# Performance work log

Hardware: AMD Instinct MI355X
Metric: run time of the kernel (lower is better)

The kernel has to match this reference:

```python
import jax, jax.numpy as jnp
import numpy as np

H = 1024      # hidden_size
V = 32000     # output_size (vocab)
BOS = 1


def setup_inputs() -> dict:
    key = jax.random.key(0)
    ks = jax.random.split(key, 12)
    B, S, T = 16, 128, 128
    s = 1.0 / np.sqrt(H)
    return {
        "encoder_outputs": jax.random.normal(ks[0], (B, S, H), jnp.float32),
        "encoder_hidden": jax.random.normal(ks[1], (1, B, H), jnp.float32),
        "tgt_tensor": jax.random.randint(ks[2], (B, T), 0, V),
        # embedding table
        "emb": jax.random.normal(ks[3], (V, H), jnp.float32) * 0.02,
        # additive attention (d2l style: Linear(..., bias=False))
        "Wq": jax.random.uniform(ks[4], (H, H), jnp.float32, -s, s),
        "Wk": jax.random.uniform(ks[5], (H, H), jnp.float32, -s, s),
        "v_att": jax.random.uniform(ks[6], (H,), jnp.float32, -s, s),
        # GRU (input size 2H): PyTorch layout W_ih [3H, 2H] (r,z,n), W_hh [3H, H]
        "W_ih": jax.random.uniform(ks[7], (3 * H, 2 * H), jnp.float32, -s, s),
        "W_hh": jax.random.uniform(ks[8], (3 * H, H), jnp.float32, -s, s),
        "b_ih": jax.random.uniform(ks[9], (3 * H,), jnp.float32, -s, s),
        "b_hh": jax.random.uniform(ks[10], (3 * H,), jnp.float32, -s, s),
        # output linear
        "W_out": jax.random.uniform(ks[11], (V, H), jnp.float32, -s, s),
        "b_out": jnp.zeros((V,), jnp.float32),
    }


def _decode(encoder_outputs, encoder_hidden, tgt_tensor,
            emb, Wq, Wk, v_att, W_ih, W_hh, b_ih, b_hh, W_out, b_out):
    B, S, _ = encoder_outputs.shape
    # decoder inputs under teacher forcing: [BOS, tgt[:, :-1]]  -> [B, T]
    dec_in = jnp.concatenate(
        [jnp.full((B, 1), BOS, dtype=tgt_tensor.dtype), tgt_tensor[:, :-1]], axis=1)
    # precompute key projection once: [B, S, H]
    kproj = jnp.einsum('bsh,gh->bsg', encoder_outputs, Wk)

    def step(h, x_t):  # h: [B,H], x_t: [B]
        e = emb[x_t]                                   # [B, H]
        q = h @ Wq.T                                   # [B, H]
        feat = jnp.tanh(q[:, None, :] + kproj)         # [B, S, H]
        scores = jnp.einsum('bsh,h->bs', feat, v_att)  # [B, S]
        w = jax.nn.softmax(scores, axis=-1)            # [B, S]
        ctx = jnp.einsum('bs,bsh->bh', w, encoder_outputs)  # [B, H]
        x = jnp.concatenate([e, ctx], axis=-1)         # [B, 2H]
        gx = x @ W_ih.T + b_ih                         # [B, 3H]
        gh = h @ W_hh.T + b_hh                         # [B, 3H]
        gx_r, gx_z, gx_n = jnp.split(gx, 3, axis=-1)
        gh_r, gh_z, gh_n = jnp.split(gh, 3, axis=-1)
        r = jax.nn.sigmoid(gx_r + gh_r)
        z = jax.nn.sigmoid(gx_z + gh_z)
        n = jnp.tanh(gx_n + r * gh_n)
        h_new = (1.0 - z) * n + z * h                  # [B, H]
        logits = h_new @ W_out.T + b_out               # [B, V]
        return h_new, (logits, w)

    h0 = encoder_hidden[0]                             # [B, H]
    hT, (logits, attw) = jax.lax.scan(step, h0, dec_in.T)  # time-major scan
    logits = jnp.transpose(logits, (1, 0, 2))          # [B, T, V]
    attw = jnp.transpose(attw, (1, 0, 2))              # [B, T, S]
    log_probs = jax.nn.log_softmax(logits, axis=-1)
    return log_probs, hT[None], attw


def reference(encoder_outputs, encoder_hidden, tgt_tensor,
              emb, Wq, Wk, v_att, W_ih, W_hh, b_ih, b_hh, W_out, b_out):
    return _decode(encoder_outputs, encoder_hidden, tgt_tensor,
                   emb, Wq, Wk, v_att, W_ih, W_hh, b_ih, b_hh, W_out, b_out)
```

## Files before the change

### kernel.cpp

```cpp
#include <hip/hip_runtime.h>

typedef unsigned short u16;
using f32x4  = __attribute__((ext_vector_type(4))) float;
using bf16x8 = __attribute__((ext_vector_type(8))) __bf16;

__device__ __forceinline__ float bf2f(u16 s){ return __builtin_bit_cast(float, (unsigned)s << 16); }
__device__ __forceinline__ float bflo(unsigned u){ return __builtin_bit_cast(float, u << 16); }
__device__ __forceinline__ float bfhi(unsigned u){ return __builtin_bit_cast(float, u & 0xffff0000u); }
__device__ __forceinline__ u16 f2bf(float f){
  unsigned u = __builtin_bit_cast(unsigned, f);
  unsigned r = u + 0x7fffu + ((u >> 16) & 1u);
  return (u16)(r >> 16);
}
__device__ __forceinline__ unsigned pk2(float x, float y){
  unsigned ux = __builtin_bit_cast(unsigned, x) + 0x8000u;
  unsigned uy = __builtin_bit_cast(unsigned, y) + 0x8000u;
  return (ux >> 16) | (uy & 0xffff0000u);
}
__device__ __forceinline__ float tanh_f(float x){ float e = __expf(2.f*x); return 1.f - 2.f/(e + 1.f); }
__device__ __forceinline__ float sigm(float x){ return 1.f/(1.f + __expf(-x)); }
__device__ __forceinline__ f32x4 mfma16(bf16x8 a, bf16x8 b, f32x4 c){
  return __builtin_amdgcn_mfma_f32_16x16x32_bf16(a, b, c, 0, 0, 0);
}
__device__ __forceinline__ bf16x8 ldg8(const u16* p){
  return __builtin_bit_cast(bf16x8, *(const uint4*)p);
}
__device__ __forceinline__ bf16x8 cvt8(const float* p){
  float4 a = *(const float4*)p, b = *(const float4*)(p + 4);
  uint4 r; r.x = pk2(a.x, a.y); r.y = pk2(a.z, a.w); r.z = pk2(b.x, b.y); r.w = pk2(b.z, b.w);
  return __builtin_bit_cast(bf16x8, r);
}
__device__ __forceinline__ void gld(const void* g, void* l){
  __builtin_amdgcn_global_load_lds(
      (const __attribute__((address_space(1))) void*)g,
      (__attribute__((address_space(3))) void*)l, 16, 0, 0);
}

__device__ __forceinline__ float coh_ld(const float* p){
  return __hip_atomic_load(p, __ATOMIC_RELAXED, __HIP_MEMORY_SCOPE_AGENT);
}
__device__ __forceinline__ void coh_st(float* p, float v){
  __hip_atomic_store(p, v, __ATOMIC_RELAXED, __HIP_MEMORY_SCOPE_AGENT);
}

template<int EPI, bool AF32, bool BF32>
__global__ __launch_bounds__(256) void gemm_bt(
    const void* __restrict__ Av, int lda,
    const void* __restrict__ Bv, int ldb,
    void* __restrict__ Cv, const float* __restrict__ bias,
    int K, int N)
{
  constexpr int ABYTES = AF32 ? 16384 : 8192;
  constexpr int BBYTES = BF32 ? 16384 : 8192;
  __shared__ __align__(16) unsigned char lsA[ABYTES];
  __shared__ __align__(16) unsigned char lsB[BBYTES];
  const int tid = threadIdx.x;
  const int wv = tid >> 6, l = tid & 63;
  const int m0 = blockIdx.y * 128, n0 = blockIdx.x * 128;
  const int wm = wv & 1, wn = wv >> 1;
  const f32x4 vzero = {0.f, 0.f, 0.f, 0.f};
  f32x4 acc[4][4];
#pragma unroll
  for (int i = 0; i < 4; ++i)
#pragma unroll
    for (int j = 0; j < 4; ++j) acc[i][j] = vzero;

  const float* gAf[4]; const u16* gAh[2]; void* dA[4];
  const float* gBf[4]; const u16* gBh[2]; void* dB[4];
  if constexpr (AF32){
    const float* A = (const float*)Av;
#pragma unroll
    for (int i = 0; i < 4; ++i){
      int e = (wv*4 + i)*64 + l;
      int kc = e >> 8, r = (e >> 1) & 127, h4 = (e & 1)*4;
      gAf[i] = A + (size_t)(m0 + r)*lda + kc*8 + h4;
      dA[i] = lsA + (wv*4 + i)*1024;
    }
  } else {
    const u16* A = (const u16*)Av;
#pragma unroll
    for (int i = 0; i < 2; ++i){
      int e = (wv*2 + i)*64 + l;
      int kc = e >> 7, r = e & 127;
      gAh[i] = A + (size_t)(m0 + r)*lda + kc*8;
      dA[i] = lsA + (wv*2 + i)*1024;
    }
  }
  if constexpr (BF32){
    const float* B = (const float*)Bv;
#pragma unroll
    for (int i = 0; i < 4; ++i){
      int e = (wv*4 + i)*64 + l;
      int kc = e >> 8, r = (e >> 1) & 127, h4 = (e & 1)*4;
      gBf[i] = B + (size_t)(n0 + r)*ldb + kc*8 + h4;
      dB[i] = lsB + (wv*4 + i)*1024;
    }
  } else {
    const u16* B = (const u16*)Bv;
#pragma unroll
    for (int i = 0; i < 2; ++i){
      int e = (wv*2 + i)*64 + l;
      int kc = e >> 7, r = e & 127;
      gBh[i] = B + (size_t)(n0 + r)*ldb + kc*8;
      dB[i] = lsB + (wv*2 + i)*1024;
    }
  }
  const int kq = l >> 4, li = l & 15;

  for (int k0 = 0; k0 < K; k0 += 32){
    __syncthreads();
    if constexpr (AF32){
#pragma unroll
      for (int i = 0; i < 4; ++i) gld(gAf[i] + k0, dA[i]);
    } else {
#pragma unroll
      for (int i = 0; i < 2; ++i) gld(gAh[i] + k0, dA[i]);
    }
    if constexpr (BF32){
#pragma unroll
      for (int i = 0; i < 4; ++i) gld(gBf[i] + k0, dB[i]);
    } else {
#pragma unroll
      for (int i = 0; i < 2; ++i) gld(gBh[i] + k0, dB[i]);
    }
    __syncthreads();
    bf16x8 aF[4], bF[4];
#pragma unroll
    for (int mi = 0; mi < 4; ++mi){
      int idx = kq*128 + wm*64 + mi*16 + li;
      if constexpr (AF32) aF[mi] = cvt8((const float*)lsA + idx*8);
      else                aF[mi] = ldg8((const u16*)lsA + idx*8);
    }
#pragma unroll
    for (int ni = 0; ni < 4; ++ni){
      int idx = kq*128 + wn*64 + ni*16 + li;
      if constexpr (BF32) bF[ni] = cvt8((const float*)lsB + idx*8);
      else                bF[ni] = ldg8((const u16*)lsB + idx*8);
    }
#pragma unroll
    for (int mi = 0; mi < 4; ++mi)
#pragma unroll
      for (int ni = 0; ni < 4; ++ni)
        acc[mi][ni] = mfma16(aF[mi], bF[ni], acc[mi][ni]);
  }

#pragma unroll
  for (int mi = 0; mi < 4; ++mi){
    const int mloc = wm*64 + mi*16 + kq*4;
#pragma unroll
    for (int ni = 0; ni < 4; ++ni){
      const int col = n0 + wn*64 + ni*16 + li;
      f32x4 v = acc[mi][ni];
      if constexpr (EPI == 1){
        float bb = bias ? bias[col] : 0.f;
        u16* C = (u16*)Cv;
#pragma unroll
        for (int r = 0; r < 4; ++r)
          C[(size_t)(m0 + mloc + r)*N + col] = f2bf(v[r] + bb);
      } else if constexpr (EPI == 2){
        float bb = bias[col];
        float* C = (float*)Cv;
#pragma unroll
        for (int r = 0; r < 4; ++r){
          int m = m0 + mloc + r;
          int orow = (m & 15)*128 + (m >> 4);
          C[(size_t)orow*N + col] = v[r] + bb;
        }
      } else {
        u16* C = (u16*)Cv;
        int m = m0 + mloc;
        int b = m >> 7, s = m & 127;
        unsigned w0 = (unsigned)f2bf(v[0]) | ((unsigned)f2bf(v[1]) << 16);
        unsigned w1 = (unsigned)f2bf(v[2]) | ((unsigned)f2bf(v[3]) << 16);
        uint2 pk; pk.x = w0; pk.y = w1;
        *(uint2*)(C + ((size_t)b*N + col)*128 + s) = pk;
      }
    }
  }
}

__global__ void cast_w2(const float* __restrict__ Wq, const float* __restrict__ Whh, u16* __restrict__ Wc2){
  int r2 = blockIdx.x;
  int ic = r2 >> 8, lr = r2 & 255;
  const float* src;
  if (lr < 64) src = Wq + (size_t)(ic*64 + lr)*1024;
  else { int gate = (lr - 64) >> 6, i = (lr - 64) & 63; src = Whh + (size_t)(gate*1024 + ic*64 + i)*1024; }
  const float4* s4 = (const float4*)src + threadIdx.x*2;
  float4 a = s4[0], c = s4[1];
  uint4 r; r.x = pk2(a.x, a.y); r.y = pk2(a.z, a.w); r.z = pk2(c.x, c.y); r.w = pk2(c.z, c.w);
  ((uint4*)(Wc2 + (size_t)r2*1024))[threadIdx.x] = r;
}

__global__ void gather_e(const int* __restrict__ tgt, const float* __restrict__ emb, u16* __restrict__ eall){
  int p = blockIdx.x;
  int t = p >> 4, b = p & 15;
  int tok = (t == 0) ? 1 : tgt[b*128 + (t - 1)];
  const float4* src = (const float4*)(emb + (size_t)tok*1024) + threadIdx.x*2;
  float4 a = src[0], c = src[1];
  uint4 r; r.x = pk2(a.x, a.y); r.y = pk2(a.z, a.w); r.z = pk2(c.x, c.y); r.w = pk2(c.z, c.w);
  ((uint4*)(eall + (size_t)p*1024))[threadIdx.x] = r;
}

__global__ void init_h(const float* __restrict__ eh, float* __restrict__ hf, int* __restrict__ bar){
  int i = blockIdx.x*256 + threadIdx.x;
  if (i < 1024) bar[i] = 0;
  hf[i] = eh[i];
}

struct RP {
  const u16 *Wc2, *kproj, *Pt, *ge;
  const float *bhh, *vatt;
  float *psc, *hf;
  u16 *hseq;
  float *outT, *attw;
  int *bar;
};

__device__ __forceinline__ void gbar(int* cnt, int target){
  __syncthreads();
  if (threadIdx.x == 0){
    __hip_atomic_fetch_add(cnt, 1, __ATOMIC_RELAXED, __HIP_MEMORY_SCOPE_AGENT);
    while (__hip_atomic_load(cnt, __ATOMIC_RELAXED, __HIP_MEMORY_SCOPE_AGENT) < target)
      __builtin_amdgcn_s_sleep(1);
  }
  __syncthreads();
}

__global__ __launch_bounds__(256) void rec_kernel(RP p){
  __shared__ float hshm[1024];
  __shared__ float qv[64];
  __shared__ float ghv[192];
  __shared__ float vv[64];
  __shared__ float sraw[128];
  __shared__ float wf[128];
  __shared__ float gcv[192];
  const int tid = threadIdx.x;
  const int blk = blockIdx.x;
  const int b = blk >> 4, ic = blk & 15;
  const int wv = tid >> 6, l = tid & 63;
  int* cnt = p.bar + b*32;
  int target = 0;

  const u16* wr = p.Wc2 + ((size_t)(ic*256 + tid))*1024;
  float badd = 0.f;
  if (tid >= 64){
    int gate = (tid - 64) >> 6, i = (tid - 64) & 63;
    badd = p.bhh[gate*1024 + ic*64 + i];
  }
  if (tid < 64) vv[tid] = p.vatt[ic*64 + tid];

  const int s_pair = tid >> 1, half = tid & 1;
  const u16* kbase = p.kproj + ((size_t)(b*128 + s_pair))*1024 + ic*64 + half*32;
  float* pscw = p.psc + (b*16 + ic)*128 + s_pair;

  float hreg = (tid < 64) ? p.hf[b*1024 + ic*64 + tid] : 0.f;

  for (int t = 0; t < 128; ++t){
    {
      const float* hfb = p.hf + b*1024 + tid*4;
      float4 hv;
      hv.x = coh_ld(hfb + 0); hv.y = coh_ld(hfb + 1);
      hv.z = coh_ld(hfb + 2); hv.w = coh_ld(hfb + 3);
      ((float4*)hshm)[tid] = hv;
    }
    __syncthreads();
    {
      float a0 = 0.f, a1 = 0.f, a2 = 0.f, a3 = 0.f;
#pragma unroll 8
      for (int k0 = 0; k0 < 1024; k0 += 8){
        uint4 u = *(const uint4*)(wr + k0);
        a0 += hshm[k0+0]*bflo(u.x) + hshm[k0+1]*bfhi(u.x);
        a1 += hshm[k0+2]*bflo(u.y) + hshm[k0+3]*bfhi(u.y);
        a2 += hshm[k0+4]*bflo(u.z) + hshm[k0+5]*bfhi(u.z);
        a3 += hshm[k0+6]*bflo(u.w) + hshm[k0+7]*bfhi(u.w);
      }
      float r = (a0 + a1) + (a2 + a3) + badd;
      if (tid < 64) qv[tid] = r; else ghv[tid - 64] = r;
    }
    __syncthreads();
    {
      float acc = 0.f;
#pragma unroll
      for (int c = 0; c < 4; ++c){
        uint4 u = *(const uint4*)(kbase + c*8);
        int j = half*32 + c*8;
        acc += vv[j+0]*tanh_f(qv[j+0] + bflo(u.x)) + vv[j+1]*tanh_f(qv[j+1] + bfhi(u.x));
        acc += vv[j+2]*tanh_f(qv[j+2] + bflo(u.y)) + vv[j+3]*tanh_f(qv[j+3] + bfhi(u.y));
        acc += vv[j+4]*tanh_f(qv[j+4] + bflo(u.z)) + vv[j+5]*tanh_f(qv[j+5] + bfhi(u.z));
        acc += vv[j+6]*tanh_f(qv[j+6] + bflo(u.w)) + vv[j+7]*tanh_f(qv[j+7] + bfhi(u.w));
      }
      acc += __shfl_xor(acc, 1);
      if (half == 0) coh_st(pscw, acc);
    }
    target += 16; gbar(cnt, target);

    if (tid < 128){
      const float* pr = p.psc + b*2048 + tid;
      float s0 = 0.f;
#pragma unroll
      for (int j = 0; j < 16; ++j) s0 += coh_ld(pr + j*128);
      sraw[tid] = s0;
    }
    __syncthreads();
    if (wv == 0){
      float x0 = sraw[l], x1 = sraw[64 + l];
      float m = fmaxf(x0, x1);
#pragma unroll
      for (int o = 32; o; o >>= 1) m = fmaxf(m, __shfl_xor(m, o));
      float e0 = __expf(x0 - m), e1 = __expf(x1 - m);
      float sm = e0 + e1;
#pragma unroll
      for (int o = 32; o; o >>= 1) sm += __shfl_xor(sm, o);
      float inv = 1.f / sm;
      wf[l] = e0*inv; wf[64 + l] = e1*inv;
    }
    __syncthreads();
    if (tid < 192){
      int gate = tid >> 6, ii = tid & 63;
      int j = gate*1024 + ic*64 + ii;
      const uint4* pr = (const uint4*)(p.Pt + ((size_t)(b*3072 + j))*128);
      float acc = 0.f;
#pragma unroll
      for (int c = 0; c < 16; ++c){
        uint4 u = pr[c];
        const float* w8 = &wf[c*8];
        acc += w8[0]*bflo(u.x) + w8[1]*bfhi(u.x)
             + w8[2]*bflo(u.y) + w8[3]*bfhi(u.y)
             + w8[4]*bflo(u.z) + w8[5]*bfhi(u.z)
             + w8[6]*bflo(u.w) + w8[7]*bfhi(u.w);
      }
      gcv[tid] = acc;
    }
    __syncthreads();
    if (tid < 64){
      int i = ic*64 + tid;
      size_t mrow = (size_t)(t*16 + b);
      const u16* gep = p.ge + mrow*3072;
      float ger = bf2f(gep[i]), gez = bf2f(gep[i + 1024]), gen = bf2f(gep[i + 2048]);
      float ghr = ghv[tid], ghz = ghv[64 + tid], ghn = ghv[128 + tid];
      float rg = sigm(ger + gcv[tid] + ghr);
      float z  = sigm(gez + gcv[64 + tid] + ghz);
      float n  = tanh_f(gen + gcv[128 + tid] + rg*ghn);
      float hn = (1.f - z)*n + z*hreg;
      hreg = hn;
      coh_st(p.hf + b*1024 + i, hn);
      p.hseq[mrow*1024 + i] = f2bf(hn);
      if (t == 127) p.outT[b*1024 + i] = hn;
    }
    if (ic == 0 && tid < 128){
      p.attw[((size_t)(b*128 + t))*128 + tid] = wf[tid];
    }
    target += 16; gbar(cnt, target);
  }
}

__global__ __launch_bounds__(256) void lse_kernel(const float* __restrict__ outp, float* __restrict__ lse){
  __shared__ float rm[256], rs[256];
  int r = blockIdx.x, tid = threadIdx.x;
  const float4* rp = (const float4*)(outp + (size_t)r*32000);
  float m = -3.0e38f, s = 0.f;
  for (int v = tid; v < 8000; v += 256){
    float4 x = rp[v];
    float mx = fmaxf(fmaxf(x.x, x.y), fmaxf(x.z, x.w));
    if (mx > m){ s *= __expf(m - mx); m = mx; }
    s += __expf(x.x - m) + __expf(x.y - m) + __expf(x.z - m) + __expf(x.w - m);
  }
  rm[tid] = m; rs[tid] = s;
  __syncthreads();
  for (int o = 128; o; o >>= 1){
    if (tid < o){
      float m2 = rm[tid + o], s2 = rs[tid + o], m1 = rm[tid], s1 = rs[tid];
      float M = fmaxf(m1, m2);
      rs[tid] = s1*__expf(m1 - M) + s2*__expf(m2 - M);
      rm[tid] = M;
    }
    __syncthreads();
  }
  if (tid == 0) lse[r] = rm[0] + __logf(rs[0]);
}

__global__ __launch_bounds__(256) void fixup_kernel(float* __restrict__ outp, const float* __restrict__ lse){
  int idx = blockIdx.x*256 + threadIdx.x;
  int r = idx / 8000;
  float L = lse[r];
  float4* p4 = (float4*)outp;
  float4 u = p4[idx];
  u.x -= L; u.y -= L; u.z -= L; u.w -= L;
  p4[idx] = u;
}

extern "C" void kernel_launch(void* const* d_in, const int* in_sizes, int n_in,
                              void* d_out, int out_size, void* d_ws, size_t ws_size,
                              hipStream_t stream) {
  (void)in_sizes; (void)n_in; (void)out_size; (void)ws_size;
  const float* eo   = (const float*)d_in[0];
  const float* eh   = (const float*)d_in[1];
  const int*   tgt  = (const int*)d_in[2];
  const float* emb  = (const float*)d_in[3];
  const float* Wq   = (const float*)d_in[4];
  const float* Wk   = (const float*)d_in[5];
  const float* vatt = (const float*)d_in[6];
  const float* Wih  = (const float*)d_in[7];
  const float* Whh  = (const float*)d_in[8];
  const float* bih  = (const float*)d_in[9];
  const float* bhh  = (const float*)d_in[10];
  const float* Wout = (const float*)d_in[11];
  const float* bout = (const float*)d_in[12];
  float* out = (float*)d_out;

  char* ws = (char*)d_ws;
  u16*  kproj = (u16*) (ws + 0);
  u16*  ge    = (u16*) (ws + 4194304);
  u16*  Pt    = (u16*) (ws + 16777216);
  u16*  eall  = (u16*) (ws + 29360128);
  u16*  hseq  = (u16*) (ws + 33554432);
  u16*  wc2   = (u16*) (ws + 37748736);
  float* hf   = (float*)(ws + 46137344);
  int*  bar   = (int*)  (ws + 46202880);
  float* psc  = (float*)(ws + 46235648);
  float* lse  = (float*)(ws + 46505984);

  float* outT = out + 65536000;
  float* attw = out + 65552384;

  cast_w2<<<4096, 128, 0, stream>>>(Wq, Whh, wc2);
  gather_e<<<2048, 128, 0, stream>>>(tgt, emb, eall);
  init_h<<<64, 256, 0, stream>>>(eh, hf, bar);

  gemm_bt<1, true, true><<<dim3(8, 16), 256, 0, stream>>>(eo, 1024, Wk, 1024, kproj, nullptr, 1024, 1024);
  gemm_bt<1, false, true><<<dim3(24, 16), 256, 0, stream>>>(eall, 1024, Wih, 2048, ge, bih, 1024, 3072);
  gemm_bt<3, true, true><<<dim3(24, 16), 256, 0, stream>>>(eo, 1024, Wih + 1024, 2048, Pt, nullptr, 1024, 3072);

  RP rp;
  rp.Wc2 = wc2; rp.kproj = kproj; rp.Pt = Pt; rp.ge = ge;
  rp.bhh = bhh; rp.vatt = vatt;
  rp.psc = psc; rp.hf = hf;
  rp.hseq = hseq; rp.outT = outT; rp.attw = attw;
  rp.bar = bar;
  void* kargs[] = { (void*)&rp };
  hipLaunchCooperativeKernel((void*)rec_kernel, dim3(256), dim3(256), kargs, 0, stream);

  gemm_bt<2, false, true><<<dim3(250, 16), 256, 0, stream>>>(hseq, 1024, Wout, 1024, out, bout, 1024, 32000);
  lse_kernel<<<2048, 256, 0, stream>>>(out, lse);
  fixup_kernel<<<64000, 256, 0, stream>>>(out, lse);
}
```

Before: 4.004 ms.

## Double recurrent kernel block size and split per-step dot products across thread pairs

The recurrent cooperative kernel moves from 256 to 512 threads per block. Each row's recurrent GEMV, attention-score slice, and context-gate dot product is now split across two or four threads and combined with shuffles. The partial-score buffer is re-laid out so each sequence position's 16 partials are contiguous, and the cross-block score sum is spread over more threads. Gate loads and output stores become nontemporal. The aim is to shorten the latency-bound serial critical path of each timestep, at the cost of extra shuffles and higher register pressure, and the barrier counter stride is widened.

After: 3.763 ms. -6.0%, faster.

```diff
diff --git a/kernel.cpp b/kernel.cpp
--- a/kernel.cpp
+++ b/kernel.cpp
@@ -226,7 +226,7 @@
   __syncthreads();
 }
 
-__global__ __launch_bounds__(256) void rec_kernel(RP p){
+__global__ __launch_bounds__(512) void rec_kernel(RP p){
   __shared__ float hshm[1024];
   __shared__ float qv[64];
   __shared__ float ghv[192];
@@ -238,68 +238,72 @@
   const int blk = blockIdx.x;
   const int b = blk >> 4, ic = blk & 15;
   const int wv = tid >> 6, l = tid & 63;
-  int* cnt = p.bar + b*32;
+  int* cnt = p.bar + b*64;
   int target = 0;
 
-  const u16* wr = p.Wc2 + ((size_t)(ic*256 + tid))*1024;
+  const int lr = tid >> 1, half = tid & 1;
+  const u16* wr = p.Wc2 + ((size_t)(ic*256 + lr))*1024 + half*512;
   float badd = 0.f;
-  if (tid >= 64){
-    int gate = (tid - 64) >> 6, i = (tid - 64) & 63;
-    badd = p.bhh[gate*1024 + ic*64 + i];
-  }
+  if (lr >= 64){ int gate = (lr - 64) >> 6, i = (lr - 64) & 63; badd = p.bhh[gate*1024 + ic*64 + i]; }
   if (tid < 64) vv[tid] = p.vatt[ic*64 + tid];
 
-  const int s_pair = tid >> 1, half = tid & 1;
-  const u16* kbase = p.kproj + ((size_t)(b*128 + s_pair))*1024 + ic*64 + half*32;
-  float* pscw = p.psc + (b*16 + ic)*128 + s_pair;
+  const int sq = tid >> 2, q4 = tid & 3;
+  const u16* kbase = p.kproj + ((size_t)(b*128 + sq))*1024 + ic*64 + q4*16;
+  float* pscw = p.psc + ((size_t)(b*128 + sq))*16 + ic;
 
   float hreg = (tid < 64) ? p.hf[b*1024 + ic*64 + tid] : 0.f;
 
   for (int t = 0; t < 128; ++t){
     {
-      const float* hfb = p.hf + b*1024 + tid*4;
-      float4 hv;
-      hv.x = coh_ld(hfb + 0); hv.y = coh_ld(hfb + 1);
-      hv.z = coh_ld(hfb + 2); hv.w = coh_ld(hfb + 3);
-      ((float4*)hshm)[tid] = hv;
+      const float* hfb = p.hf + b*1024 + tid*2;
+      float2 hv; hv.x = coh_ld(hfb); hv.y = coh_ld(hfb + 1);
+      ((float2*)hshm)[tid] = hv;
     }
     __syncthreads();
     {
+      const float* hb = hshm + half*512;
       float a0 = 0.f, a1 = 0.f, a2 = 0.f, a3 = 0.f;
 #pragma unroll 8
-      for (int k0 = 0; k0 < 1024; k0 += 8){
+      for (int k0 = 0; k0 < 512; k0 += 8){
         uint4 u = *(const uint4*)(wr + k0);
-        a0 += hshm[k0+0]*bflo(u.x) + hshm[k0+1]*bfhi(u.x);
-        a1 += hshm[k0+2]*bflo(u.y) + hshm[k0+3]*bfhi(u.y);
-        a2 += hshm[k0+4]*bflo(u.z) + hshm[k0+5]*bfhi(u.z);
-        a3 += hshm[k0+6]*bflo(u.w) + hshm[k0+7]*bfhi(u.w);
+        a0 += hb[k0+0]*bflo(u.x) + hb[k0+1]*bfhi(u.x);
+        a1 += hb[k0+2]*bflo(u.y) + hb[k0+3]*bfhi(u.y);
+        a2 += hb[k0+4]*bflo(u.z) + hb[k0+5]*bfhi(u.z);
+        a3 += hb[k0+6]*bflo(u.w) + hb[k0+7]*bfhi(u.w);
       }
-      float r = (a0 + a1) + (a2 + a3) + badd;
-      if (tid < 64) qv[tid] = r; else ghv[tid - 64] = r;
+      float rsum = (a0 + a1) + (a2 + a3);
+      rsum += __shfl_xor(rsum, 1);
+      if (half == 0){
+        float r = rsum + badd;
+        if (lr < 64) qv[lr] = r; else ghv[lr - 64] = r;
+      }
     }
     __syncthreads();
     {
+      uint4 u0 = *(const uint4*)(kbase);
+      uint4 u1 = *(const uint4*)(kbase + 8);
+      int j = q4*16;
       float acc = 0.f;
-#pragma unroll
-      for (int c = 0; c < 4; ++c){
-        uint4 u = *(const uint4*)(kbase + c*8);
-        int j = half*32 + c*8;
-        acc += vv[j+0]*tanh_f(qv[j+0] + bflo(u.x)) + vv[j+1]*tanh_f(qv[j+1] + bfhi(u.x));
-        acc += vv[j+2]*tanh_f(qv[j+2] + bflo(u.y)) + vv[j+3]*tanh_f(qv[j+3] + bfhi(u.y));
-        acc += vv[j+4]*tanh_f(qv[j+4] + bflo(u.z)) + vv[j+5]*tanh_f(qv[j+5] + bfhi(u.z));
-        acc += vv[j+6]*tanh_f(qv[j+6] + bflo(u.w)) + vv[j+7]*tanh_f(qv[j+7] + bfhi(u.w));
-      }
+      acc += vv[j+0]*tanh_f(qv[j+0] + bflo(u0.x)) + vv[j+1]*tanh_f(qv[j+1] + bfhi(u0.x));
+      acc += vv[j+2]*tanh_f(qv[j+2] + bflo(u0.y)) + vv[j+3]*tanh_f(qv[j+3] + bfhi(u0.y));
+      acc += vv[j+4]*tanh_f(qv[j+4] + bflo(u0.z)) + vv[j+5]*tanh_f(qv[j+5] + bfhi(u0.z));
+      acc += vv[j+6]*tanh_f(qv[j+6] + bflo(u0.w)) + vv[j+7]*tanh_f(qv[j+7] + bfhi(u0.w));
+      acc += vv[j+8]*tanh_f(qv[j+8] + bflo(u1.x)) + vv[j+9]*tanh_f(qv[j+9] + bfhi(u1.x));
+      acc += vv[j+10]*tanh_f(qv[j+10] + bflo(u1.y)) + vv[j+11]*tanh_f(qv[j+11] + bfhi(u1.y));
+      acc += vv[j+12]*tanh_f(qv[j+12] + bflo(u1.z)) + vv[j+13]*tanh_f(qv[j+13] + bfhi(u1.z));
+      acc += vv[j+14]*tanh_f(qv[j+14] + bflo(u1.w)) + vv[j+15]*tanh_f(qv[j+15] + bfhi(u1.w));
       acc += __shfl_xor(acc, 1);
-      if (half == 0) coh_st(pscw, acc);
+      acc += __shfl_xor(acc, 2);
+      if (q4 == 0) coh_st(pscw, acc);
     }
     target += 16; gbar(cnt, target);
 
-    if (tid < 128){
-      const float* pr = p.psc + b*2048 + tid;
-      float s0 = 0.f;
-#pragma unroll
-      for (int j = 0; j < 16; ++j) s0 += coh_ld(pr + j*128);
-      sraw[tid] = s0;
+    {
+      const float* pr = p.psc + ((size_t)(b*128 + sq))*16 + q4*4;
+      float s0 = coh_ld(pr) + coh_ld(pr + 1) + coh_ld(pr + 2) + coh_ld(pr + 3);
+      s0 += __shfl_xor(s0, 1);
+      s0 += __shfl_xor(s0, 2);
+      if (q4 == 0) sraw[sq] = s0;
     }
     __syncthreads();
     if (wv == 0){
@@ -315,40 +319,42 @@
       wf[l] = e0*inv; wf[64 + l] = e1*inv;
     }
     __syncthreads();
-    if (tid < 192){
-      int gate = tid >> 6, ii = tid & 63;
-      int j = gate*1024 + ic*64 + ii;
-      const uint4* pr = (const uint4*)(p.Pt + ((size_t)(b*3072 + j))*128);
+    if (tid < 384){
+      int jj = tid >> 1, hf2 = tid & 1;
+      int j = (jj >> 6)*1024 + ic*64 + (jj & 63);
+      const uint4* pr2 = (const uint4*)(p.Pt + ((size_t)(b*3072 + j))*128) + hf2*8;
       float acc = 0.f;
 #pragma unroll
-      for (int c = 0; c < 16; ++c){
-        uint4 u = pr[c];
-        const float* w8 = &wf[c*8];
+      for (int c = 0; c < 8; ++c){
+        uint4 u = pr2[c];
+        const float* w8 = &wf[(hf2*8 + c)*8];
         acc += w8[0]*bflo(u.x) + w8[1]*bfhi(u.x)
              + w8[2]*bflo(u.y) + w8[3]*bfhi(u.y)
              + w8[4]*bflo(u.z) + w8[5]*bfhi(u.z)
              + w8[6]*bflo(u.w) + w8[7]*bfhi(u.w);
       }
-      gcv[tid] = acc;
+      acc += __shfl_xor(acc, 1);
+      if (hf2 == 0) gcv[jj] = acc;
     }
     __syncthreads();
     if (tid < 64){
       int i = ic*64 + tid;
       size_t mrow = (size_t)(t*16 + b);
       const u16* gep = p.ge + mrow*3072;
-      float ger = bf2f(gep[i]), gez = bf2f(gep[i + 1024]), gen = bf2f(gep[i + 2048]);
-      float ghr = ghv[tid], ghz = ghv[64 + tid], ghn = ghv[128 + tid];
-      float rg = sigm(ger + gcv[tid] + ghr);
-      float z  = sigm(gez + gcv[64 + tid] + ghz);
-      float n  = tanh_f(gen + gcv[128 + tid] + rg*ghn);
+      float ger = bf2f(__builtin_nontemporal_load(gep + i));
+      float gez = bf2f(__builtin_nontemporal_load(gep + i + 1024));
+      float gen = bf2f(__builtin_nontemporal_load(gep + i + 2048));
+      float rg = sigm(ger + gcv[tid] + ghv[tid]);
+      float z  = sigm(gez + gcv[64 + tid] + ghv[64 + tid]);
+      float n  = tanh_f(gen + gcv[128 + tid] + rg*ghv[128 + tid]);
       float hn = (1.f - z)*n + z*hreg;
       hreg = hn;
       coh_st(p.hf + b*1024 + i, hn);
-      p.hseq[mrow*1024 + i] = f2bf(hn);
+      __builtin_nontemporal_store(f2bf(hn), p.hseq + mrow*1024 + i);
       if (t == 127) p.outT[b*1024 + i] = hn;
     }
     if (ic == 0 && tid < 128){
-      p.attw[((size_t)(b*128 + t))*128 + tid] = wf[tid];
+      __builtin_nontemporal_store(wf[tid], p.attw + ((size_t)(b*128 + t))*128 + tid);
     }
     target += 16; gbar(cnt, target);
   }
@@ -438,7 +444,7 @@
   rp.hseq = hseq; rp.outT = outT; rp.attw = attw;
   rp.bar = bar;
   void* kargs[] = { (void*)&rp };
-  hipLaunchCooperativeKernel((void*)rec_kernel, dim3(256), dim3(256), kargs, 0, stream);
+  hipLaunchCooperativeKernel((void*)rec_kernel, dim3(256), dim3(512), kargs, 0, stream);
 
   gemm_bt<2, false, true><<<dim3(250, 16), 256, 0, stream>>>(hseq, 1024, Wout, 1024, out, bout, 1024, 32000);
   lse_kernel<<<2048, 256, 0, stream>>>(out, lse);
```
